# Kernel optimization log

Hardware: AMD Instinct MI355X
Metric: run time of the kernel (lower is better)

The kernel has to match this reference:

```python
import jax, jax.numpy as jnp
import numpy as np

TOP_K = 8
N_EXPERTS = 64
HIDDEN = 4096


def setup_inputs() -> dict:
    key = jax.random.key(0)
    k1, k2 = jax.random.split(key)
    hidden_states = jax.random.normal(k1, (4, 4096, HIDDEN), dtype=jnp.float32)
    # kaiming_uniform_(a=sqrt(5)) on a (64, 4096) weight -> U(-b, b), b = sqrt(6/((1+5)*4096)) = 1/sqrt(4096)
    bound = 1.0 / np.sqrt(HIDDEN)
    weight = jax.random.uniform(k2, (N_EXPERTS, HIDDEN), dtype=jnp.float32,
                                minval=-bound, maxval=bound)
    return {"hidden_states": hidden_states, "weight": weight}


def reference(hidden_states, weight):
    bsz, seq_len, h = hidden_states.shape
    x = hidden_states.reshape(-1, h)                       # [T, H]
    logits = jnp.einsum('th,eh->te', x, weight)            # [T, E]
    scores = jax.nn.softmax(logits, axis=-1)
    topk_weight, topk_idx = jax.lax.top_k(scores, TOP_K)   # [T, K]
    denom = jnp.sum(topk_weight, axis=-1, keepdims=True) + 1e-20
    topk_weight = topk_weight / denom
    topk_weight = topk_weight.reshape(bsz, seq_len, TOP_K)
    topk_idx = topk_idx.reshape(bsz, seq_len, TOP_K)
    # training-time aux loss (seq_aux path): histogram of argmax expert * mean prob
    probs = scores                                         # softmax(logits)
    top1 = jnp.argmax(probs, axis=-1)                      # [T]
    counts = jnp.zeros((N_EXPERTS,), dtype=jnp.float32).at[top1].add(1.0)
    route_prob = jnp.mean(probs, axis=0)                   # [E]
    route_frac = counts / jnp.sum(counts)
    aux_loss = jnp.sum(route_prob * route_frac) * N_EXPERTS
    return topk_idx, topk_weight, aux_loss
```

## Files before the change

### kernel.cpp

```cpp
#include <hip/hip_runtime.h>
#include <hip/hip_bf16.h>

#define TOKS 16384
#define HID  4096
#define NEXP 64
#define EPS  1e-4f

#define WS_FLAGCNT  128
#define WS_FLAGLIST 192
#define WS_BPACK    16576

typedef __attribute__((ext_vector_type(8))) short short8_t;
typedef __attribute__((ext_vector_type(4))) float f32x4;

static __device__ __forceinline__ unsigned short f2bf_rn(float x) {
    unsigned u = __builtin_bit_cast(unsigned, x);
    u = (u + 0x7fffu + ((u >> 16) & 1u)) >> 16;
    return (unsigned short)u;
}
static __device__ __forceinline__ float bf2f(unsigned short h) {
    return __builtin_bit_cast(float, (unsigned)h << 16);
}
static __device__ __forceinline__ void gl2lds16(const void* g, void* l) {
    __builtin_amdgcn_global_load_lds(
        (const __attribute__((address_space(1))) unsigned int*)g,
        (__attribute__((address_space(3))) unsigned int*)l, 16, 0, 0);
}

__global__ void moe_prep(const float* __restrict__ W, unsigned short* __restrict__ Bpk,
                         float* __restrict__ wsf) {
    const int idx = blockIdx.x * blockDim.x + threadIdx.x;
    if (idx < 192) wsf[idx] = 0.0f;
    if (idx >= NEXP * HID) return;
    const int n = idx >> 12;
    const int k = idx & 4095;
    const float w = W[idx];
    const unsigned short hi = f2bf_rn(w);
    const unsigned short lo = f2bf_rn(w - bf2f(hi));
    const int kt   = k >> 5;
    const int nt   = n >> 4;
    const int lane = (n & 15) | (((k >> 3) & 3) << 4);
    const int j    = k & 7;
    const int dst  = (((kt << 2) + nt) << 10) + (lane << 3) + j;
    Bpk[dst]       = hi;
    Bpk[dst + 512] = lo;
}

__global__ __launch_bounds__(512, 1)
void moe_fused(const float* __restrict__ X, const unsigned short* __restrict__ Bpk,
               float* __restrict__ out, float* __restrict__ wsf) {
    __shared__ __align__(16) float xbuf[4][64][64];
    __shared__ __align__(16) unsigned short bbuf[4][8192];
    float (*L)[68] = (float (*)[68])&xbuf[0][0][0];

    const int tid  = threadIdx.x;
    const int lane = tid & 63;
    const int w    = tid >> 6;
    const int mt   = w & 3;
    const int nh   = w >> 2;
    const int g    = lane >> 4;
    const int tok0 = blockIdx.x * 64;

    f32x4 acc[2];
    acc[0] = (f32x4){0.f, 0.f, 0.f, 0.f};
    acc[1] = (f32x4){0.f, 0.f, 0.f, 0.f};

    #define STAGE(bf, ss)                                                              \
    {                                                                                  \
        const int k0_ = (ss) << 6;                                                     \
        _Pragma("unroll")                                                              \
        for (int i = 0; i < 2; ++i) {                                                  \
            const int rg = (w << 3) + (i << 2) + g;                                    \
            const int ck = (lane & 15) ^ (rg & 15);                                    \
            gl2lds16(X + (size_t)(tok0 + rg) * HID + k0_ + (ck << 2),                  \
                     (void*)&xbuf[bf][(w << 3) + (i << 2)][0]);                        \
        }                                                                              \
        _Pragma("unroll")                                                              \
        for (int j = 0; j < 2; ++j) {                                                  \
            const int c1k = (w << 1) + j;                                              \
            gl2lds16((const char*)Bpk + ((size_t)(ss) << 14) + (c1k << 10) + (lane << 4), \
                     (void*)((char*)&bbuf[bf][0] + (c1k << 10)));                      \
        }                                                                              \
    }

    STAGE(0, 0);
    STAGE(1, 1);

    const int tr  = (mt << 4) + (lane & 15);
    const int rsw = lane & 15;

    for (int s = 0; s < 64; ++s) {
        const int cur = s & 3;
        {
            const int ss = (s + 2 < 64) ? (s + 2) : 63;
            STAGE((s + 2) & 3, ss);
        }
        asm volatile("s_waitcnt vmcnt(8)" ::: "memory");
        __builtin_amdgcn_s_barrier();
        __builtin_amdgcn_sched_barrier(0);

        const char* ab = (const char*)&xbuf[cur][tr][0];
        const char* bb = (const char*)&bbuf[cur][0];
        #pragma unroll
        for (int ktl = 0; ktl < 2; ++ktl) {
            const int cl = (ktl << 3) + (g << 1);
            const float4 a0 = *(const float4*)(ab + ((cl ^ rsw) << 4));
            const float4 a1 = *(const float4*)(ab + (((cl + 1) ^ rsw) << 4));
            const float xv[8] = {a0.x, a0.y, a0.z, a0.w, a1.x, a1.y, a1.z, a1.w};
            short8_t ah, al;
            #pragma unroll
            for (int j = 0; j < 8; ++j) {
                const unsigned u = __builtin_bit_cast(unsigned, xv[j]);
                ah[j] = (short)(u >> 16);
                const float hif = __builtin_bit_cast(float, u & 0xFFFF0000u);
                al[j] = (short)(__builtin_bit_cast(unsigned, xv[j] - hif) >> 16);
            }
            #pragma unroll
            for (int ntl = 0; ntl < 2; ++ntl) {
                const char* bp = bb + (((ktl << 2) + (nh << 1) + ntl) << 11) + (lane << 4);
                const short8_t bh = *(const short8_t*)bp;
                const short8_t bl = *(const short8_t*)(bp + 1024);
                acc[ntl] = __builtin_amdgcn_mfma_f32_16x16x32_bf16(ah, bh, acc[ntl], 0, 0, 0);
                acc[ntl] = __builtin_amdgcn_mfma_f32_16x16x32_bf16(al, bh, acc[ntl], 0, 0, 0);
                acc[ntl] = __builtin_amdgcn_mfma_f32_16x16x32_bf16(ah, bl, acc[ntl], 0, 0, 0);
            }
        }
    }
    asm volatile("s_waitcnt vmcnt(0)" ::: "memory");
    __syncthreads();

    #pragma unroll
    for (int ntl = 0; ntl < 2; ++ntl)
        #pragma unroll
        for (int r = 0; r < 4; ++r)
            L[(mt << 4) + (g << 2) + r][(nh << 5) + (ntl << 4) + (lane & 15)] = acc[ntl][r];
    __syncthreads();

    float* outIdx = out;
    float* outW   = out + TOKS * 8;
    int* flagcnt  = (int*)wsf + WS_FLAGCNT;
    int* flaglist = (int*)wsf + WS_FLAGLIST;

    float rp = 0.f;
    #pragma unroll
    for (int tt = 0; tt < 8; ++tt) {
        const int tl = (w << 3) + tt;
        const float lg = L[tl][lane];

        float v = lg; int idx = lane;
        #pragma unroll
        for (int size = 2; size <= 64; size <<= 1) {
            #pragma unroll
            for (int str = size >> 1; str > 0; str >>= 1) {
                const float ov = __shfl_xor(v, str, 64);
                const int   oi = __shfl_xor(idx, str, 64);
                const bool pb = (ov > v) || (ov == v && oi < idx);
                const bool keepFirst = ((lane & str) == 0) == ((lane & size) == 0);
                if (pb == keepFirst) { v = ov; idx = oi; }
            }
        }

        const float m = __shfl(v, 0, 64);
        const float p = __expf(lg - m);
        float sdenom = p;
        #pragma unroll
        for (int o = 32; o; o >>= 1) sdenom += __shfl_xor(sdenom, o, 64);
        const float inv_s = 1.0f / sdenom;
        rp += p * inv_s;

        const float wkv = __expf(v - m) * inv_s;
        float d8 = (lane < 8) ? wkv : 0.f;
        #pragma unroll
        for (int o = 1; o < 8; o <<= 1) d8 += __shfl_xor(d8, o, 64);
        const float invd = 1.0f / (d8 + 1e-20f);
        const float nv = __shfl_down(v, 1, 64);
        const bool flg = __any(lane < 8 && (v - nv) < EPS);

        const int gtok = tok0 + tl;
        if (lane < 8) {
            outIdx[(size_t)gtok * 8 + lane] = (float)idx;
            outW[(size_t)gtok * 8 + lane]   = wkv * invd;
        }
        if (lane == 0) {
            atomicAdd(&wsf[NEXP + idx], 1.0f);
            if (flg) {
                const int pos = atomicAdd(flagcnt, 1);
                if (pos < TOKS) flaglist[pos] = gtok;
            }
        }
    }
    atomicAdd(&wsf[lane], rp);
    #undef STAGE
}

__global__ __launch_bounds__(256, 2)
void moe_fix(const float* __restrict__ X, const float* __restrict__ W,
             float* __restrict__ out, float* __restrict__ wsf) {
    __shared__ double red[256];
    const int tid = threadIdx.x;
    const int e   = tid & 63;
    const int kc  = tid >> 6;
    const int nf  = min(*((int*)wsf + WS_FLAGCNT), TOKS);
    const int* flaglist = (const int*)wsf + WS_FLAGLIST;
    float* outIdx = out;
    float* outW   = out + TOKS * 8;

    for (int fi = blockIdx.x; fi < nf; fi += gridDim.x) {
        const int tok = flaglist[fi];
        const float* xrow = X + (size_t)tok * HID + kc * 1024;
        const float* wrow = W + (size_t)e  * HID + kc * 1024;
        double part = 0.0;
        for (int j = 0; j < 1024; j += 4) {
            const float4 xv = *(const float4*)(xrow + j);
            const float4 wv = *(const float4*)(wrow + j);
            part = fma((double)xv.x, (double)wv.x, part);
            part = fma((double)xv.y, (double)wv.y, part);
            part = fma((double)xv.z, (double)wv.z, part);
            part = fma((double)xv.w, (double)wv.w, part);
        }
        red[tid] = part;
        __syncthreads();
        if (tid < 64) {
            const double lg = ((red[tid] + red[64 + tid]) + red[128 + tid]) + red[192 + tid];
            const float lgf = (float)lg;
            float m = lgf;
            #pragma unroll
            for (int o = 32; o; o >>= 1) m = fmaxf(m, __shfl_xor(m, o, 64));
            const float p = __expf(lgf - m);
            float s = p;
            #pragma unroll
            for (int o = 32; o; o >>= 1) s += __shfl_xor(s, o, 64);
            const float inv_s = 1.0f / s;

            double v = lg;
            double bw[8]; int ik[8];
            #pragma unroll
            for (int k = 0; k < 8; ++k) {
                double bv = v; int bi = tid;
                #pragma unroll
                for (int o = 32; o; o >>= 1) {
                    const double ov = __shfl_xor(bv, o, 64);
                    const int    oi = __shfl_xor(bi, o, 64);
                    if (ov > bv || (ov == bv && oi < bi)) { bv = ov; bi = oi; }
                }
                bw[k] = bv; ik[k] = bi;
                if (tid == bi) v = -1.0e300;
            }
            float wk[8]; float denom = 1e-20f;
            #pragma unroll
            for (int k = 0; k < 8; ++k) {
                wk[k] = __expf((float)bw[k] - m) * inv_s; denom += wk[k];
            }
            const float invd = 1.0f / denom;
            const size_t base = (size_t)tok * 8;
            const int oldtop = (int)outIdx[base];
            if (tid < 8) {
                outIdx[base + tid] = (float)ik[tid];
                outW[base + tid]   = wk[tid] * invd;
            }
            if (tid == 0 && ik[0] != oldtop) {
                atomicAdd(&wsf[NEXP + oldtop], -1.0f);
                atomicAdd(&wsf[NEXP + ik[0]],  1.0f);
            }
        }
        __syncthreads();
    }
}

__global__ void moe_final(const float* __restrict__ wsf, float* __restrict__ out) {
    const int e = threadIdx.x;
    float v = wsf[e] * wsf[NEXP + e];
    #pragma unroll
    for (int o = 32; o; o >>= 1) v += __shfl_xor(v, o, 64);
    if (e == 0)
        out[2 * TOKS * 8] = v * (64.0f / ((float)TOKS * (float)TOKS));
}

__global__ void moe_init(float* __restrict__ wsf, int n) {
    const int i = blockIdx.x * blockDim.x + threadIdx.x;
    if (i < n) wsf[i] = 0.0f;
}

__global__ void moe_w_cvt(const float* __restrict__ W, double* __restrict__ Wd) {
    const int i = blockIdx.x * blockDim.x + threadIdx.x;
    if (i < NEXP * HID) Wd[i] = (double)W[i];
}

__global__ __launch_bounds__(512, 2)
void moe_mono(const float* __restrict__ X, const double* __restrict__ Wd,
              float* __restrict__ out, float* __restrict__ wsf) {
    __shared__ double xs[64][66];
    __shared__ double L2[64][65];
    const int tid  = threadIdx.x;
    const int lane = tid & 63;
    const int wid  = __builtin_amdgcn_readfirstlane(tid >> 6);
    const int tok0 = blockIdx.x * 64;
    double acc[8] = {0., 0., 0., 0., 0., 0., 0., 0.};
    for (int h0 = 0; h0 < HID; h0 += 64) {
        #pragma unroll
        for (int i = 0; i < 8; ++i) {
            const int li = tid + i * 512;
            xs[li >> 6][li & 63] = (double)X[((size_t)(tok0 + (li >> 6)) << 12) + (h0 + (li & 63))];
        }
        __syncthreads();
        const double* wchunk = Wd + (((size_t)(wid << 3)) << 12) + h0;
        #pragma unroll 2
        for (int hh = 0; hh < 64; hh += 2) {
            const double2 xv = *(const double2*)&xs[lane][hh];
            #pragma unroll
            for (int e = 0; e < 8; ++e) {
                const double* wr = wchunk + (((size_t)e) << 12) + hh;
                acc[e] = fma(xv.x, wr[0], acc[e]);
                acc[e] = fma(xv.y, wr[1], acc[e]);
            }
        }
        __syncthreads();
    }
    #pragma unroll
    for (int e = 0; e < 8; ++e) L2[lane][(wid << 3) + e] = acc[e];
    __syncthreads();
    float* outIdx = out;
    float* outW   = out + (TOKS * 8);
    float rp = 0.0f;
    for (int tt = 0; tt < 8; ++tt) {
        const int t = (wid << 3) + tt;
        const double lg = L2[t][lane];
        const float lgf = (float)lg;
        float m = lgf;
        #pragma unroll
        for (int o = 32; o; o >>= 1) m = fmaxf(m, __shfl_xor(m, o, 64));
        const float p = __expf(lgf - m);
        float s = p;
        #pragma unroll
        for (int o = 32; o; o >>= 1) s += __shfl_xor(s, o, 64);
        const float inv_s = 1.0f / s;
        rp += p * inv_s;
        double v = lg;
        float wk[8]; int ik[8];
        #pragma unroll
        for (int k = 0; k < 8; ++k) {
            double bv = v; int bi = lane;
            #pragma unroll
            for (int o = 32; o; o >>= 1) {
                const double ov = __shfl_xor(bv, o, 64);
                const int    oi = __shfl_xor(bi, o, 64);
                if (ov > bv || (ov == bv && oi < bi)) { bv = ov; bi = oi; }
            }
            wk[k] = __expf((float)bv - m) * inv_s; ik[k] = bi;
            if (lane == bi) v = -1.0e300;
        }
        if (lane == 0) {
            const float denom = (((wk[0]+wk[1])+(wk[2]+wk[3])) +
                                 ((wk[4]+wk[5])+(wk[6]+wk[7]))) + 1e-20f;
            const float invd = 1.0f / denom;
            const size_t base = ((size_t)(tok0 + t)) << 3;
            #pragma unroll
            for (int k = 0; k < 8; ++k) {
                outIdx[base + k] = (float)ik[k];
                outW[base + k]   = wk[k] * invd;
            }
            atomicAdd(&wsf[NEXP + ik[0]], 1.0f);
        }
    }
    atomicAdd(&wsf[lane], rp);
}

extern "C" void kernel_launch(void* const* d_in, const int* in_sizes, int n_in,
                              void* d_out, int out_size, void* d_ws, size_t ws_size,
                              hipStream_t stream) {
    const float* X = (const float*)d_in[0];
    const float* W = (const float*)d_in[1];
    float* out = (float*)d_out;
    float* wsf = (float*)d_ws;

    const size_t need = 4ull * WS_BPACK + 2ull * 524288;

    if (ws_size >= need) {
        unsigned short* Bpk = (unsigned short*)(wsf + WS_BPACK);
        moe_prep<<<(NEXP * HID + 255) / 256, 256, 0, stream>>>(W, Bpk, wsf);
        moe_fused<<<TOKS / 64, 512, 0, stream>>>(X, Bpk, out, wsf);
        moe_fix<<<256, 256, 0, stream>>>(X, W, out, wsf);
        moe_final<<<1, 64, 0, stream>>>(wsf, out);
    } else {
        double* Wd = (double*)d_ws;
        float* wsf2 = (float*)(Wd + NEXP * HID);
        moe_w_cvt<<<(NEXP * HID + 255) / 256, 256, 0, stream>>>(W, Wd);
        moe_init<<<1, 256, 0, stream>>>(wsf2, 128);
        moe_mono<<<TOKS / 64, 512, 0, stream>>>(X, Wd, out, wsf2);
        moe_final<<<1, 64, 0, stream>>>(wsf2, out);
    }
}
```

Measured before the change: 212.1 us.

## Split fused GEMM+topk into separate GEMM and top-k kernels via logits buffer

Defuses the router kernel: the GEMM kernel now writes logits to a workspace buffer and a new lightweight top-k kernel reads them back, computing softmax stats and 9 sequential argmax shuffles instead of a full 64-wide bitonic sort. This shortens the GEMM kernel's epilogue tail and spreads the top-k work over more, smaller blocks. The cost is an extra kernel launch plus a 4 MB write and read of logits, and it needs a larger workspace.

Result: slower. 246.2 us (+16.1%).

```diff
diff --git a/kernel.cpp b/kernel.cpp
--- a/kernel.cpp
+++ b/kernel.cpp
@@ -9,6 +9,7 @@
 #define WS_FLAGCNT  128
 #define WS_FLAGLIST 192
 #define WS_BPACK    16576
+#define WS_PBASE    278720
 
 typedef __attribute__((ext_vector_type(8))) short short8_t;
 typedef __attribute__((ext_vector_type(4))) float f32x4;
@@ -47,8 +48,8 @@
 }
 
 __global__ __launch_bounds__(512, 1)
-void moe_fused(const float* __restrict__ X, const unsigned short* __restrict__ Bpk,
-               float* __restrict__ out, float* __restrict__ wsf) {
+void moe_gemm(const float* __restrict__ X, const unsigned short* __restrict__ Bpk,
+              float* __restrict__ P) {
     __shared__ __align__(16) float xbuf[4][64][64];
     __shared__ __align__(16) unsigned short bbuf[4][8192];
     float (*L)[68] = (float (*)[68])&xbuf[0][0][0];
@@ -135,7 +136,24 @@
         for (int r = 0; r < 4; ++r)
             L[(mt << 4) + (g << 2) + r][(nh << 5) + (ntl << 4) + (lane & 15)] = acc[ntl][r];
     __syncthreads();
-
+    {
+        const int row = tid >> 3;
+        const int c0  = (tid & 7) << 3;
+        float* dst = P + (size_t)(tok0 + row) * NEXP + c0;
+        const float* src = &L[row][c0];
+        *(float4*)dst       = *(const float4*)src;
+        *(float4*)(dst + 4) = *(const float4*)(src + 4);
+    }
+    #undef STAGE
+}
+
+__global__ __launch_bounds__(256, 4)
+void moe_topk(const float* __restrict__ P, float* __restrict__ out,
+              float* __restrict__ wsf) {
+    const int tid  = threadIdx.x;
+    const int lane = tid & 63;
+    const int wid  = tid >> 6;
+    const int tok0 = blockIdx.x * 16;
     float* outIdx = out;
     float* outW   = out + TOKS * 8;
     int* flagcnt  = (int*)wsf + WS_FLAGCNT;
@@ -143,54 +161,56 @@
 
     float rp = 0.f;
     #pragma unroll
-    for (int tt = 0; tt < 8; ++tt) {
-        const int tl = (w << 3) + tt;
-        const float lg = L[tl][lane];
-
-        float v = lg; int idx = lane;
-        #pragma unroll
-        for (int size = 2; size <= 64; size <<= 1) {
-            #pragma unroll
-            for (int str = size >> 1; str > 0; str >>= 1) {
-                const float ov = __shfl_xor(v, str, 64);
-                const int   oi = __shfl_xor(idx, str, 64);
-                const bool pb = (ov > v) || (ov == v && oi < idx);
-                const bool keepFirst = ((lane & str) == 0) == ((lane & size) == 0);
-                if (pb == keepFirst) { v = ov; idx = oi; }
-            }
-        }
-
-        const float m = __shfl(v, 0, 64);
+    for (int tt = 0; tt < 4; ++tt) {
+        const int tok = tok0 + wid * 4 + tt;
+        const float lg = P[(size_t)tok * NEXP + lane];
+
+        float m = lg;
+        #pragma unroll
+        for (int o = 32; o; o >>= 1) m = fmaxf(m, __shfl_xor(m, o, 64));
         const float p = __expf(lg - m);
-        float sdenom = p;
-        #pragma unroll
-        for (int o = 32; o; o >>= 1) sdenom += __shfl_xor(sdenom, o, 64);
-        const float inv_s = 1.0f / sdenom;
+        float s = p;
+        #pragma unroll
+        for (int o = 32; o; o >>= 1) s += __shfl_xor(s, o, 64);
+        const float inv_s = 1.0f / s;
         rp += p * inv_s;
 
-        const float wkv = __expf(v - m) * inv_s;
-        float d8 = (lane < 8) ? wkv : 0.f;
-        #pragma unroll
-        for (int o = 1; o < 8; o <<= 1) d8 += __shfl_xor(d8, o, 64);
-        const float invd = 1.0f / (d8 + 1e-20f);
-        const float nv = __shfl_down(v, 1, 64);
-        const bool flg = __any(lane < 8 && (v - nv) < EPS);
-
-        const int gtok = tok0 + tl;
+        float v = lg;
+        float lw[9]; int ik[9];
+        #pragma unroll
+        for (int k = 0; k < 9; ++k) {
+            float bv = v; int bi = lane;
+            #pragma unroll
+            for (int o = 32; o; o >>= 1) {
+                const float ov = __shfl_xor(bv, o, 64);
+                const int   oi = __shfl_xor(bi, o, 64);
+                if (ov > bv || (ov == bv && oi < bi)) { bv = ov; bi = oi; }
+            }
+            lw[k] = bv; ik[k] = bi;
+            if (lane == bi) v = -3.0e38f;
+        }
+        float mingap = 3.0e38f;
+        #pragma unroll
+        for (int k = 0; k < 8; ++k) mingap = fminf(mingap, lw[k] - lw[k + 1]);
+
+        float wk[8]; float denom = 1e-20f;
+        #pragma unroll
+        for (int k = 0; k < 8; ++k) { wk[k] = __expf(lw[k] - m) * inv_s; denom += wk[k]; }
+        const float invd = 1.0f / denom;
+        const size_t base = (size_t)tok * 8;
         if (lane < 8) {
-            outIdx[(size_t)gtok * 8 + lane] = (float)idx;
-            outW[(size_t)gtok * 8 + lane]   = wkv * invd;
+            outIdx[base + lane] = (float)ik[lane];
+            outW[base + lane]   = wk[lane] * invd;
         }
         if (lane == 0) {
-            atomicAdd(&wsf[NEXP + idx], 1.0f);
-            if (flg) {
+            atomicAdd(&wsf[NEXP + ik[0]], 1.0f);
+            if (mingap < EPS) {
                 const int pos = atomicAdd(flagcnt, 1);
-                if (pos < TOKS) flaglist[pos] = gtok;
+                if (pos < TOKS) flaglist[pos] = tok;
             }
         }
     }
     atomicAdd(&wsf[lane], rp);
-    #undef STAGE
 }
 
 __global__ __launch_bounds__(256, 2)
@@ -373,12 +393,14 @@
     float* out = (float*)d_out;
     float* wsf = (float*)d_ws;
 
-    const size_t need = 4ull * WS_BPACK + 2ull * 524288;
+    const size_t need = 4ull * (WS_PBASE + (size_t)TOKS * NEXP);
 
     if (ws_size >= need) {
         unsigned short* Bpk = (unsigned short*)(wsf + WS_BPACK);
+        float* P = wsf + WS_PBASE;
         moe_prep<<<(NEXP * HID + 255) / 256, 256, 0, stream>>>(W, Bpk, wsf);
-        moe_fused<<<TOKS / 64, 512, 0, stream>>>(X, Bpk, out, wsf);
+        moe_gemm<<<TOKS / 64, 512, 0, stream>>>(X, Bpk, P);
+        moe_topk<<<TOKS / 16, 256, 0, stream>>>(P, out, wsf);
         moe_fix<<<256, 256, 0, stream>>>(X, W, out, wsf);
         moe_final<<<1, 64, 0, stream>>>(wsf, out);
     } else {
```

## Deepen LDS pipeline to 8 stages with smaller 32-wide K tiles

Applied to the files above, without the earlier changes.

Halves the K-step per stage from 64 to 32 and doubles the iteration count, while raising the ring of LDS buffers from 4 to 8 and prefetching 6 stages ahead. Each warp now issues one X load and one B load per stage, with a new XOR swizzle for 8 chunks per row. The aim is to keep more global loads in flight to hide HBM latency on this bandwidth-bound GEMV-like gating matmul. The cost is twice as many barriers per K, with less MFMA work between them.

Result: slower. 242.6 us (+14.4%).

```diff
diff --git a/kernel.cpp b/kernel.cpp
--- a/kernel.cpp
+++ b/kernel.cpp
@@ -49,9 +49,9 @@
 __global__ __launch_bounds__(512, 1)
 void moe_fused(const float* __restrict__ X, const unsigned short* __restrict__ Bpk,
                float* __restrict__ out, float* __restrict__ wsf) {
-    __shared__ __align__(16) float xbuf[4][64][64];
-    __shared__ __align__(16) unsigned short bbuf[4][8192];
-    float (*L)[68] = (float (*)[68])&xbuf[0][0][0];
+    __shared__ __align__(16) char xbuf[8][8192];
+    __shared__ __align__(16) char bbuf[8][8192];
+    float (*L)[68] = (float (*)[68])&xbuf[0][0];
 
     const int tid  = threadIdx.x;
     const int lane = tid & 63;
@@ -59,71 +59,57 @@
     const int mt   = w & 3;
     const int nh   = w >> 2;
     const int g    = lane >> 4;
+    const int r    = lane & 15;
     const int tok0 = blockIdx.x * 64;
 
     f32x4 acc[2];
     acc[0] = (f32x4){0.f, 0.f, 0.f, 0.f};
     acc[1] = (f32x4){0.f, 0.f, 0.f, 0.f};
 
+    const int xrow = (w << 3) + (lane >> 3);
+    const int xchk = (lane & 7) ^ ((lane >> 3) & 7);
+    const size_t xsrc = (size_t)(tok0 + xrow) * HID + (xchk << 2);
+    const char* BpkB = (const char*)Bpk;
+
     #define STAGE(bf, ss)                                                              \
     {                                                                                  \
-        const int k0_ = (ss) << 6;                                                     \
-        _Pragma("unroll")                                                              \
-        for (int i = 0; i < 2; ++i) {                                                  \
-            const int rg = (w << 3) + (i << 2) + g;                                    \
-            const int ck = (lane & 15) ^ (rg & 15);                                    \
-            gl2lds16(X + (size_t)(tok0 + rg) * HID + k0_ + (ck << 2),                  \
-                     (void*)&xbuf[bf][(w << 3) + (i << 2)][0]);                        \
-        }                                                                              \
-        _Pragma("unroll")                                                              \
-        for (int j = 0; j < 2; ++j) {                                                  \
-            const int c1k = (w << 1) + j;                                              \
-            gl2lds16((const char*)Bpk + ((size_t)(ss) << 14) + (c1k << 10) + (lane << 4), \
-                     (void*)((char*)&bbuf[bf][0] + (c1k << 10)));                      \
-        }                                                                              \
-    }
-
-    STAGE(0, 0);
-    STAGE(1, 1);
-
-    const int tr  = (mt << 4) + (lane & 15);
-    const int rsw = lane & 15;
-
-    for (int s = 0; s < 64; ++s) {
-        const int cur = s & 3;
-        {
-            const int ss = (s + 2 < 64) ? (s + 2) : 63;
-            STAGE((s + 2) & 3, ss);
-        }
-        asm volatile("s_waitcnt vmcnt(8)" ::: "memory");
+        gl2lds16(X + xsrc + ((ss) << 5), (void*)(&xbuf[bf][0] + (w << 10)));           \
+        gl2lds16(BpkB + ((size_t)(ss) << 13) + (w << 10) + (lane << 4),                \
+                 (void*)(&bbuf[bf][0] + (w << 10)));                                   \
+    }
+
+    #pragma unroll
+    for (int i = 0; i < 6; ++i) STAGE(i, i);
+
+    for (int s = 0; s < 128; ++s) {
+        const int cur = s & 7;
+        const int ss = (s + 6 < 128) ? (s + 6) : 127;
+        STAGE((s + 6) & 7, ss);
+        asm volatile("s_waitcnt vmcnt(12)" ::: "memory");
         __builtin_amdgcn_s_barrier();
         __builtin_amdgcn_sched_barrier(0);
 
-        const char* ab = (const char*)&xbuf[cur][tr][0];
-        const char* bb = (const char*)&bbuf[cur][0];
-        #pragma unroll
-        for (int ktl = 0; ktl < 2; ++ktl) {
-            const int cl = (ktl << 3) + (g << 1);
-            const float4 a0 = *(const float4*)(ab + ((cl ^ rsw) << 4));
-            const float4 a1 = *(const float4*)(ab + (((cl + 1) ^ rsw) << 4));
-            const float xv[8] = {a0.x, a0.y, a0.z, a0.w, a1.x, a1.y, a1.z, a1.w};
-            short8_t ah, al;
-            #pragma unroll
-            for (int j = 0; j < 8; ++j) {
-                const unsigned u = __builtin_bit_cast(unsigned, xv[j]);
-                ah[j] = (short)(u >> 16);
-                const float hif = __builtin_bit_cast(float, u & 0xFFFF0000u);
-                al[j] = (short)(__builtin_bit_cast(unsigned, xv[j] - hif) >> 16);
-            }
-            #pragma unroll
-            for (int ntl = 0; ntl < 2; ++ntl) {
-                const char* bp = bb + (((ktl << 2) + (nh << 1) + ntl) << 11) + (lane << 4);
-                const short8_t bh = *(const short8_t*)bp;
-                const short8_t bl = *(const short8_t*)(bp + 1024);
-                acc[ntl] = __builtin_amdgcn_mfma_f32_16x16x32_bf16(ah, bh, acc[ntl], 0, 0, 0);
-                acc[ntl] = __builtin_amdgcn_mfma_f32_16x16x32_bf16(al, bh, acc[ntl], 0, 0, 0);
-                acc[ntl] = __builtin_amdgcn_mfma_f32_16x16x32_bf16(ah, bl, acc[ntl], 0, 0, 0);
-            }
+        const char* ab = &xbuf[cur][0] + (((mt << 4) + r) << 7);
+        const char* bb = &bbuf[cur][0];
+        const float4 a0 = *(const float4*)(ab + ((((g << 1))     ^ (r & 7)) << 4));
+        const float4 a1 = *(const float4*)(ab + ((((g << 1) | 1) ^ (r & 7)) << 4));
+        const float xv[8] = {a0.x, a0.y, a0.z, a0.w, a1.x, a1.y, a1.z, a1.w};
+        short8_t ah, al;
+        #pragma unroll
+        for (int j = 0; j < 8; ++j) {
+            const unsigned u = __builtin_bit_cast(unsigned, xv[j]);
+            ah[j] = (short)(u >> 16);
+            const float hif = __builtin_bit_cast(float, u & 0xFFFF0000u);
+            al[j] = (short)(__builtin_bit_cast(unsigned, xv[j] - hif) >> 16);
+        }
+        #pragma unroll
+        for (int ntl = 0; ntl < 2; ++ntl) {
+            const char* bp = bb + (((nh << 1) + ntl) << 11) + (lane << 4);
+            const short8_t bh = *(const short8_t*)bp;
+            const short8_t bl = *(const short8_t*)(bp + 1024);
+            acc[ntl] = __builtin_amdgcn_mfma_f32_16x16x32_bf16(ah, bh, acc[ntl], 0, 0, 0);
+            acc[ntl] = __builtin_amdgcn_mfma_f32_16x16x32_bf16(al, bh, acc[ntl], 0, 0, 0);
+            acc[ntl] = __builtin_amdgcn_mfma_f32_16x16x32_bf16(ah, bl, acc[ntl], 0, 0, 0);
         }
     }
     asm volatile("s_waitcnt vmcnt(0)" ::: "memory");
@@ -132,8 +118,8 @@
     #pragma unroll
     for (int ntl = 0; ntl < 2; ++ntl)
         #pragma unroll
-        for (int r = 0; r < 4; ++r)
-            L[(mt << 4) + (g << 2) + r][(nh << 5) + (ntl << 4) + (lane & 15)] = acc[ntl][r];
+        for (int rr = 0; rr < 4; ++rr)
+            L[(mt << 4) + (g << 2) + rr][(nh << 5) + (ntl << 4) + r] = acc[ntl][rr];
     __syncthreads();
 
     float* outIdx = out;
```

## Split fused gate kernel into producer and consumer warp roles

Applied to the files above, without the earlier changes.

The block grows from 8 to 12 waves. The 4 extra waves only issue the global-to-LDS loads for X and the packed weights, and the 8 original waves only run the MFMA compute, with the two groups synchronised by per-stage barriers. The aim is to take load issue and waitcnt stalls off the compute waves so memory traffic overlaps the split-bf16 MFMAs. The cost is extra wave slots and register pressure from the larger launch bound. Correctness now depends on barrier counts matching between the two roles, and the compute waves no longer wait on vmcnt themselves.

New measurement: 201.8 us, median of 2. -4.9%, faster.

```diff
diff --git a/kernel.cpp b/kernel.cpp
--- a/kernel.cpp
+++ b/kernel.cpp
@@ -46,94 +46,106 @@
     Bpk[dst + 512] = lo;
 }
 
-__global__ __launch_bounds__(512, 1)
+__global__ __launch_bounds__(768, 1)
 void moe_fused(const float* __restrict__ X, const unsigned short* __restrict__ Bpk,
                float* __restrict__ out, float* __restrict__ wsf) {
-    __shared__ __align__(16) float xbuf[4][64][64];
-    __shared__ __align__(16) unsigned short bbuf[4][8192];
-    float (*L)[68] = (float (*)[68])&xbuf[0][0][0];
+    __shared__ __align__(16) char xbuf[4][16384];
+    __shared__ __align__(16) char bbuf[4][16384];
+    float (*L)[68] = (float (*)[68])&xbuf[0][0];
 
     const int tid  = threadIdx.x;
     const int lane = tid & 63;
     const int w    = tid >> 6;
-    const int mt   = w & 3;
-    const int nh   = w >> 2;
-    const int g    = lane >> 4;
     const int tok0 = blockIdx.x * 64;
 
     f32x4 acc[2];
     acc[0] = (f32x4){0.f, 0.f, 0.f, 0.f};
     acc[1] = (f32x4){0.f, 0.f, 0.f, 0.f};
 
-    #define STAGE(bf, ss)                                                              \
-    {                                                                                  \
-        const int k0_ = (ss) << 6;                                                     \
-        _Pragma("unroll")                                                              \
-        for (int i = 0; i < 2; ++i) {                                                  \
-            const int rg = (w << 3) + (i << 2) + g;                                    \
-            const int ck = (lane & 15) ^ (rg & 15);                                    \
-            gl2lds16(X + (size_t)(tok0 + rg) * HID + k0_ + (ck << 2),                  \
-                     (void*)&xbuf[bf][(w << 3) + (i << 2)][0]);                        \
-        }                                                                              \
-        _Pragma("unroll")                                                              \
-        for (int j = 0; j < 2; ++j) {                                                  \
-            const int c1k = (w << 1) + j;                                              \
-            gl2lds16((const char*)Bpk + ((size_t)(ss) << 14) + (c1k << 10) + (lane << 4), \
-                     (void*)((char*)&bbuf[bf][0] + (c1k << 10)));                      \
-        }                                                                              \
-    }
-
-    STAGE(0, 0);
-    STAGE(1, 1);
-
-    const int tr  = (mt << 4) + (lane & 15);
-    const int rsw = lane & 15;
-
-    for (int s = 0; s < 64; ++s) {
-        const int cur = s & 3;
-        {
+    if (w >= 8) {
+        const int p = w - 8;
+        size_t xsrc[4]; int xdst[4];
+        #pragma unroll
+        for (int j = 0; j < 4; ++j) {
+            const int i  = (p << 2) + j;
+            const int rg = (i << 2) + (lane >> 4);
+            const int ck = (lane & 15) ^ (rg & 15);
+            xsrc[j] = (size_t)(tok0 + rg) * HID + (ck << 2);
+            xdst[j] = i << 10;
+        }
+        const char* BpkB = (const char*)Bpk;
+        #define PSTAGE(bf, ss)                                                         \
+        {                                                                              \
+            const int k0_ = (ss) << 6;                                                 \
+            _Pragma("unroll")                                                          \
+            for (int j = 0; j < 4; ++j)                                                \
+                gl2lds16(X + xsrc[j] + k0_, (void*)(&xbuf[bf][0] + xdst[j]));          \
+            _Pragma("unroll")                                                          \
+            for (int j = 0; j < 4; ++j) {                                              \
+                const int c1k = (p << 2) + j;                                          \
+                gl2lds16(BpkB + ((size_t)(ss) << 14) + (c1k << 10) + (lane << 4),      \
+                         (void*)(&bbuf[bf][0] + (c1k << 10)));                         \
+            }                                                                          \
+        }
+        PSTAGE(0, 0);
+        PSTAGE(1, 1);
+        for (int s = 0; s < 64; ++s) {
             const int ss = (s + 2 < 64) ? (s + 2) : 63;
-            STAGE((s + 2) & 3, ss);
-        }
-        asm volatile("s_waitcnt vmcnt(8)" ::: "memory");
-        __builtin_amdgcn_s_barrier();
-        __builtin_amdgcn_sched_barrier(0);
-
-        const char* ab = (const char*)&xbuf[cur][tr][0];
-        const char* bb = (const char*)&bbuf[cur][0];
-        #pragma unroll
-        for (int ktl = 0; ktl < 2; ++ktl) {
-            const int cl = (ktl << 3) + (g << 1);
-            const float4 a0 = *(const float4*)(ab + ((cl ^ rsw) << 4));
-            const float4 a1 = *(const float4*)(ab + (((cl + 1) ^ rsw) << 4));
-            const float xv[8] = {a0.x, a0.y, a0.z, a0.w, a1.x, a1.y, a1.z, a1.w};
-            short8_t ah, al;
-            #pragma unroll
-            for (int j = 0; j < 8; ++j) {
-                const unsigned u = __builtin_bit_cast(unsigned, xv[j]);
-                ah[j] = (short)(u >> 16);
-                const float hif = __builtin_bit_cast(float, u & 0xFFFF0000u);
-                al[j] = (short)(__builtin_bit_cast(unsigned, xv[j] - hif) >> 16);
-            }
-            #pragma unroll
-            for (int ntl = 0; ntl < 2; ++ntl) {
-                const char* bp = bb + (((ktl << 2) + (nh << 1) + ntl) << 11) + (lane << 4);
-                const short8_t bh = *(const short8_t*)bp;
-                const short8_t bl = *(const short8_t*)(bp + 1024);
-                acc[ntl] = __builtin_amdgcn_mfma_f32_16x16x32_bf16(ah, bh, acc[ntl], 0, 0, 0);
-                acc[ntl] = __builtin_amdgcn_mfma_f32_16x16x32_bf16(al, bh, acc[ntl], 0, 0, 0);
-                acc[ntl] = __builtin_amdgcn_mfma_f32_16x16x32_bf16(ah, bl, acc[ntl], 0, 0, 0);
-            }
-        }
-    }
-    asm volatile("s_waitcnt vmcnt(0)" ::: "memory");
+            PSTAGE((s + 2) & 3, ss);
+            asm volatile("s_waitcnt vmcnt(8)" ::: "memory");
+            __builtin_amdgcn_s_barrier();
+        }
+        asm volatile("s_waitcnt vmcnt(0)" ::: "memory");
+        #undef PSTAGE
+    } else {
+        const int mt = w & 3;
+        const int nh = w >> 2;
+        const int g  = lane >> 4;
+        const int tr = (mt << 4) + (lane & 15);
+        const int rsw = lane & 15;
+        for (int s = 0; s < 64; ++s) {
+            __builtin_amdgcn_s_barrier();
+            __builtin_amdgcn_sched_barrier(0);
+            const int cur = s & 3;
+            const char* ab = &xbuf[cur][0] + (tr << 8);
+            const char* bb = &bbuf[cur][0];
+            #pragma unroll
+            for (int ktl = 0; ktl < 2; ++ktl) {
+                const int cl = (ktl << 3) + (g << 1);
+                const float4 a0 = *(const float4*)(ab + ((cl ^ rsw) << 4));
+                const float4 a1 = *(const float4*)(ab + (((cl + 1) ^ rsw) << 4));
+                const float xv[8] = {a0.x, a0.y, a0.z, a0.w, a1.x, a1.y, a1.z, a1.w};
+                short8_t ah, al;
+                #pragma unroll
+                for (int j = 0; j < 8; ++j) {
+                    const unsigned u = __builtin_bit_cast(unsigned, xv[j]);
+                    ah[j] = (short)(u >> 16);
+                    const float hif = __builtin_bit_cast(float, u & 0xFFFF0000u);
+                    al[j] = (short)(__builtin_bit_cast(unsigned, xv[j] - hif) >> 16);
+                }
+                #pragma unroll
+                for (int ntl = 0; ntl < 2; ++ntl) {
+                    const char* bp = bb + (((ktl << 2) + (nh << 1) + ntl) << 11) + (lane << 4);
+                    const short8_t bh = *(const short8_t*)bp;
+                    const short8_t bl = *(const short8_t*)(bp + 1024);
+                    acc[ntl] = __builtin_amdgcn_mfma_f32_16x16x32_bf16(ah, bh, acc[ntl], 0, 0, 0);
+                    acc[ntl] = __builtin_amdgcn_mfma_f32_16x16x32_bf16(al, bh, acc[ntl], 0, 0, 0);
+                    acc[ntl] = __builtin_amdgcn_mfma_f32_16x16x32_bf16(ah, bl, acc[ntl], 0, 0, 0);
+                }
+            }
+            __builtin_amdgcn_sched_barrier(0);
+        }
+    }
     __syncthreads();
 
-    #pragma unroll
-    for (int ntl = 0; ntl < 2; ++ntl)
-        #pragma unroll
-        for (int r = 0; r < 4; ++r)
-            L[(mt << 4) + (g << 2) + r][(nh << 5) + (ntl << 4) + (lane & 15)] = acc[ntl][r];
+    if (w < 8) {
+        const int mt = w & 3, nh = w >> 2, g = lane >> 4;
+        #pragma unroll
+        for (int ntl = 0; ntl < 2; ++ntl)
+            #pragma unroll
+            for (int rr = 0; rr < 4; ++rr)
+                L[(mt << 4) + (g << 2) + rr][(nh << 5) + (ntl << 4) + (lane & 15)] = acc[ntl][rr];
+    }
     __syncthreads();
 
     float* outIdx = out;
@@ -141,56 +153,57 @@
     int* flagcnt  = (int*)wsf + WS_FLAGCNT;
     int* flaglist = (int*)wsf + WS_FLAGLIST;
 
-    float rp = 0.f;
-    #pragma unroll
-    for (int tt = 0; tt < 8; ++tt) {
-        const int tl = (w << 3) + tt;
-        const float lg = L[tl][lane];
-
-        float v = lg; int idx = lane;
-        #pragma unroll
-        for (int size = 2; size <= 64; size <<= 1) {
-            #pragma unroll
-            for (int str = size >> 1; str > 0; str >>= 1) {
-                const float ov = __shfl_xor(v, str, 64);
-                const int   oi = __shfl_xor(idx, str, 64);
-                const bool pb = (ov > v) || (ov == v && oi < idx);
-                const bool keepFirst = ((lane & str) == 0) == ((lane & size) == 0);
-                if (pb == keepFirst) { v = ov; idx = oi; }
-            }
-        }
-
-        const float m = __shfl(v, 0, 64);
-        const float p = __expf(lg - m);
-        float sdenom = p;
-        #pragma unroll
-        for (int o = 32; o; o >>= 1) sdenom += __shfl_xor(sdenom, o, 64);
-        const float inv_s = 1.0f / sdenom;
-        rp += p * inv_s;
-
-        const float wkv = __expf(v - m) * inv_s;
-        float d8 = (lane < 8) ? wkv : 0.f;
-        #pragma unroll
-        for (int o = 1; o < 8; o <<= 1) d8 += __shfl_xor(d8, o, 64);
-        const float invd = 1.0f / (d8 + 1e-20f);
-        const float nv = __shfl_down(v, 1, 64);
-        const bool flg = __any(lane < 8 && (v - nv) < EPS);
-
-        const int gtok = tok0 + tl;
-        if (lane < 8) {
-            outIdx[(size_t)gtok * 8 + lane] = (float)idx;
-            outW[(size_t)gtok * 8 + lane]   = wkv * invd;
-        }
-        if (lane == 0) {
-            atomicAdd(&wsf[NEXP + idx], 1.0f);
-            if (flg) {
-                const int pos = atomicAdd(flagcnt, 1);
-                if (pos < TOKS) flaglist[pos] = gtok;
-            }
-        }
-    }
-    atomicAdd(&wsf[lane], rp);
-    #undef STAGE
+    if (w < 8) {
+        float rp = 0.f;
+        #pragma unroll
+        for (int tt = 0; tt < 8; ++tt) {
+            const int tl = (w << 3) + tt;
+            const float lg = L[tl][lane];
+
+            float v = lg; int idx = lane;
+            #pragma unroll
+            for (int size = 2; size <= 64; size <<= 1) {
+                #pragma unroll
+                for (int str = size >> 1; str > 0; str >>= 1) {
+                    const float ov = __shfl_xor(v, str, 64);
+                    const int   oi = __shfl_xor(idx, str, 64);
+                    const bool pb = (ov > v) || (ov == v && oi < idx);
+                    const bool keepFirst = ((lane & str) == 0) == ((lane & size) == 0);
+                    if (pb == keepFirst) { v = ov; idx = oi; }
+                }
+            }
+
+            const float m = __shfl(v, 0, 64);
+            const float p = __expf(lg - m);
+            float sdenom = p;
+            #pragma unroll
+            for (int o = 32; o; o >>= 1) sdenom += __shfl_xor(sdenom, o, 64);
+            const float inv_s = 1.0f / sdenom;
+            rp += p * inv_s;
+
+            const float wkv = __expf(v - m) * inv_s;
+            float d8 = (lane < 8) ? wkv : 0.f;
+            #pragma unroll
+            for (int o = 1; o < 8; o <<= 1) d8 += __shfl_xor(d8, o, 64);
+            const float invd = 1.0f / (d8 + 1e-20f);
+            const float nv = __shfl_down(v, 1, 64);
+            const bool flg = __any(lane < 8 && (v - nv) < EPS);
+
+            const int gtok = tok0 + tl;
+            if (lane < 8) {
+                outIdx[(size_t)gtok * 8 + lane] = (float)idx;
+                outW[(size_t)gtok * 8 + lane]   = wkv * invd;
+            }
+            if (lane == 0) {
+                atomicAdd(&wsf[NEXP + idx], 1.0f);
+                if (flg) {
+                    const int pos = atomicAdd(flagcnt, 1);
+                    if (pos < TOKS) flaglist[pos] = gtok;
+                }
+            }
+        }
+        atomicAdd(&wsf[lane], rp);
+    }
 }
 
 __global__ __launch_bounds__(256, 2)
@@ -378,7 +391,7 @@
     if (ws_size >= need) {
         unsigned short* Bpk = (unsigned short*)(wsf + WS_BPACK);
         moe_prep<<<(NEXP * HID + 255) / 256, 256, 0, stream>>>(W, Bpk, wsf);
-        moe_fused<<<TOKS / 64, 512, 0, stream>>>(X, Bpk, out, wsf);
+        moe_fused<<<TOKS / 64, 768, 0, stream>>>(X, Bpk, out, wsf);
         moe_fix<<<256, 256, 0, stream>>>(X, W, out, wsf);
         moe_final<<<1, 64, 0, stream>>>(wsf, out);
     } else {
```
